# Performance work log

Hardware: AMD Instinct MI355X
Metric: run time of the kernel (lower is better)

The kernel has to match this reference:

```python
import jax, jax.numpy as jnp
import numpy as np

B, N, F, K, O = 4, 4096, 32, 6, 128


def setup_inputs() -> dict:
    key = jax.random.key(0)
    k1, k2, k3, k4 = jax.random.split(key, 4)
    x = jax.random.normal(k1, (B, N, F), dtype=jnp.float32)
    # dense per-batch (normalized-Laplacian-like) operator; scaled for stable recurrence
    L = jax.random.normal(k2, (B, N, N), dtype=jnp.float32) / np.float32(np.sqrt(N))
    # per-order projection weights lins[k]: in -> out  (stored [K, F, O])
    W = jax.random.normal(k3, (K, F, O), dtype=jnp.float32) * 0.1
    # per-order scalar 1x1 'theta' weights lins_theta[k]
    theta = jax.random.normal(k4, (K,), dtype=jnp.float32) * 0.1
    return {"x": x, "L": L, "W": W, "theta": theta}


def reference(x, L, W, theta):
    # Chebyshev recurrence: T0 = x, T1 = L@x, T_k = 2 L@T_{k-1} - T_{k-2}
    # Each order: elementwise scalar theta_k (the 1x1 Linear) then Linear(F->O), summed.
    k_orders = W.shape[0]
    x0 = x                                                   # [B,N,F]
    out = theta[0] * jnp.einsum('bnf,fo->bno', x0, W[0])     # [B,N,O]
    if k_orders > 1:
        x1 = jnp.matmul(L, x0)                               # [B,N,F]
        out = out + theta[1] * jnp.einsum('bnf,fo->bno', x1, W[1])
    for k in range(2, k_orders):
        x2 = 2.0 * jnp.matmul(L, x1) - x0
        out = out + theta[k] * jnp.einsum('bnf,fo->bno', x2, W[k])
        x0, x1 = x1, x2
    return out
```

## Files before the change

kernel.cpp:

```cpp
#include <hip/hip_runtime.h>

#define N4 4096
#define FF 32
#define KK 6
#define OO 128
#define BB 4

typedef __attribute__((ext_vector_type(8))) short  short8;
typedef __attribute__((ext_vector_type(4))) float  f32x4;
typedef __attribute__((ext_vector_type(4))) int    i32x4;
typedef __attribute__((ext_vector_type(2))) unsigned int u32x2;

__device__ __forceinline__ float b2f(unsigned short h) {
    union { float f; unsigned u; } v; v.u = ((unsigned)h) << 16; return v.f;
}
__device__ __forceinline__ unsigned short f2b(float f) {
    union { float f; unsigned u; } v; v.f = f;
    unsigned r = (v.u + 0x7FFFu + ((v.u >> 16) & 1u)) >> 16;
    return (unsigned short)r;
}

__device__ __forceinline__ long tb_idx(int b, int ks, int half, int lane) {
    return ((((long)b * 128 + ks) * 2 + half) * 64 + lane) * 8;
}

__global__ __launch_bounds__(256) void make_wc(const float* __restrict__ W,
                                               const float* __restrict__ theta,
                                               unsigned short* __restrict__ Wc) {
    int idx = blockIdx.x * 256 + threadIdx.x;
    int k = idx >> 12;
    Wc[idx] = f2b(theta[k] * W[idx]);
}

__global__ __launch_bounds__(256) void x_to_t(const float* __restrict__ x,
                                              unsigned short* __restrict__ T0) {
    __shared__ __align__(16) unsigned short Ol[32][72];
    int tid = threadIdx.x, bid = blockIdx.x;
    int b = bid >> 6; int nc = bid & 63; long n0 = (long)nc * 64;
    int nl = tid >> 2, fg = (tid & 3) * 8;
    const float* src = x + ((long)b * N4 + n0 + nl) * FF + fg;
    f32x4 v0 = *(const f32x4*)src;
    f32x4 v1 = *(const f32x4*)(src + 4);
#pragma unroll
    for (int e = 0; e < 4; ++e) {
        Ol[fg + e][nl]     = f2b(v0[e]);
        Ol[fg + 4 + e][nl] = f2b(v1[e]);
    }
    __syncthreads();
    int ks_l = tid >> 7, half = (tid >> 6) & 1, lane = tid & 63;
    int quad = lane >> 4, l16 = lane & 15;
    int f = half * 16 + l16, nloc = ks_l * 32 + quad * 8;
    *(i32x4*)(T0 + tb_idx(b, nc * 2 + ks_l, half, lane)) = *(const i32x4*)&Ol[f][nloc];
}

__device__ __forceinline__ void split_reduce_store(const float (*Pr)[2][64][4],
                                                   int tid, int b, int ms,
                                                   const unsigned short* __restrict__ Tpp,
                                                   unsigned short* __restrict__ Tout,
                                                   float a, float c) {
    if (tid >= 64) return;
    int half = tid >> 5, qi = (tid >> 4) & 1, l16 = tid & 15;
    f32x4 sA = {0.f, 0.f, 0.f, 0.f}, sB = {0.f, 0.f, 0.f, 0.f};
#pragma unroll
    for (int ss = 0; ss < 4; ++ss) {
        f32x4 va = *(const f32x4*)&Pr[ss][half][qi * 32 + l16][0];
        f32x4 vb = *(const f32x4*)&Pr[ss][half][qi * 32 + 16 + l16][0];
#pragma unroll
        for (int e = 0; e < 4; ++e) { sA[e] += va[e]; sB[e] += vb[e]; }
    }
    float vals[8] = {sA[0], sA[1], sA[2], sA[3], sB[0], sB[1], sB[2], sB[3]};
    int lane_o = ((ms & 1) * 2 + qi) * 16 + l16;
    long oidx = tb_idx(b, ms >> 1, half, lane_o);
    i32x4 pk;
    if (Tpp) {
        short8 tv = *(const short8*)(Tpp + oidx);
#pragma unroll
        for (int p = 0; p < 4; ++p)
            pk[p] = (unsigned)f2b(a * vals[2 * p]     + c * b2f((unsigned short)tv[2 * p]))
                  | ((unsigned)f2b(a * vals[2 * p + 1] + c * b2f((unsigned short)tv[2 * p + 1])) << 16);
    } else {
#pragma unroll
        for (int p = 0; p < 4; ++p)
            pk[p] = (unsigned)f2b(a * vals[2 * p])
                  | ((unsigned)f2b(a * vals[2 * p + 1]) << 16);
    }
    *(i32x4*)(Tout + oidx) = pk;
}

__global__ __launch_bounds__(256) void gemm_pass1(const float* __restrict__ L,
                                                  unsigned short* __restrict__ Lb,
                                                  const unsigned short* __restrict__ Tb0,
                                                  unsigned short* __restrict__ Tout) {
    __shared__ __align__(16) unsigned short Sw[4][2][2][64][8];
    __shared__ __align__(16) float Pr[4][2][64][4];
    int tid = threadIdx.x, bid = blockIdx.x;
    int b = bid >> 8, ms = bid & 255;
    int w = tid >> 6, lane = tid & 63, l16 = lane & 15;
    int rgrp = lane >> 4;
    const float* Ls = L + ((long)b * N4 + ms * 16 + rgrp) * N4 + (long)w * 1024 + l16 * 4;
    int ks_loc_w = l16 >> 3, quad_w = (l16 >> 1) & 3, e0 = (l16 & 1) * 4;
    const unsigned short* Bbase = Tb0 + tb_idx(b, w * 32, 0, lane);
    unsigned short* LbBase = Lb + (((long)(b * 256 + ms) * 128 + w * 32) * 64 + lane) * 8;

    f32x4 acc0 = {0.f,0.f,0.f,0.f}, acc1 = {0.f,0.f,0.f,0.f};
    f32x4 v[4], vn[4];
#pragma unroll
    for (int j = 0; j < 4; ++j) v[j] = *(const f32x4*)(Ls + (long)j * 4 * N4);

    for (int it = 0; it < 16; ++it) {
        if (it + 1 < 16) {
#pragma unroll
            for (int j = 0; j < 4; ++j)
                vn[j] = *(const f32x4*)(Ls + (long)j * 4 * N4 + (it + 1) * 64);
        }
        short8 b00 = *(const short8*)(Bbase + (long)(it * 2 + 0) * 1024);
        short8 b01 = *(const short8*)(Bbase + (long)(it * 2 + 0) * 1024 + 512);
        short8 b10 = *(const short8*)(Bbase + (long)(it * 2 + 1) * 1024);
        short8 b11 = *(const short8*)(Bbase + (long)(it * 2 + 1) * 1024 + 512);
        unsigned short* Sb = &Sw[w][it & 1][0][0][0];
#pragma unroll
        for (int j = 0; j < 4; ++j) {
            u32x2 pk;
            pk[0] = (unsigned)f2b(v[j][0]) | ((unsigned)f2b(v[j][1]) << 16);
            pk[1] = (unsigned)f2b(v[j][2]) | ((unsigned)f2b(v[j][3]) << 16);
            int lane_o = quad_w * 16 + j * 4 + rgrp;
            *(u32x2*)(Sb + (ks_loc_w * 64 + lane_o) * 8 + e0) = pk;
        }
#pragma unroll
        for (int h = 0; h < 2; ++h) {
            short8 af = *(const short8*)(Sb + (h * 64 + lane) * 8);
            *(short8*)(LbBase + (long)(it * 2 + h) * 512) = af;
            acc0 = __builtin_amdgcn_mfma_f32_16x16x32_bf16(af, h ? b10 : b00, acc0, 0, 0, 0);
            acc1 = __builtin_amdgcn_mfma_f32_16x16x32_bf16(af, h ? b11 : b01, acc1, 0, 0, 0);
        }
#pragma unroll
        for (int j = 0; j < 4; ++j) v[j] = vn[j];
    }
    *(f32x4*)&Pr[w][0][lane][0] = acc0;
    *(f32x4*)&Pr[w][1][lane][0] = acc1;
    __syncthreads();
    split_reduce_store(Pr, tid, b, ms, nullptr, Tout, 1.f, 0.f);
}

__global__ __launch_bounds__(256) void gemm_frag(const unsigned short* __restrict__ Lb,
                                                 const unsigned short* __restrict__ Tb,
                                                 const unsigned short* __restrict__ Tpp,
                                                 unsigned short* __restrict__ Tout,
                                                 float a, float c) {
    __shared__ __align__(16) float Pr[4][2][64][4];
    int tid = threadIdx.x, bid = blockIdx.x;
    int b = bid >> 8, ms = bid & 255;
    int s = tid >> 6, lane = tid & 63;
    const unsigned short* Ap = Lb + (((long)(b * 256 + ms) * 128 + s * 32) * 64 + lane) * 8;
    const unsigned short* Bp = Tb + tb_idx(b, s * 32, 0, lane);

    f32x4 acc0 = {0.f,0.f,0.f,0.f}, acc1 = {0.f,0.f,0.f,0.f};
    short8 Ar[4], B0r[4], B1r[4];
#pragma unroll
    for (int i = 0; i < 4; ++i) {
        Ar[i]  = *(const short8*)(Ap + (long)i * 512);
        B0r[i] = *(const short8*)(Bp + (long)i * 1024);
        B1r[i] = *(const short8*)(Bp + (long)i * 1024 + 512);
    }
#pragma unroll 4
    for (int ks = 0; ks < 32; ++ks) {
        int sl = ks & 3;
        short8 aa = Ar[sl], b0 = B0r[sl], b1 = B1r[sl];
        if (ks + 4 < 32) {
            Ar[sl]  = *(const short8*)(Ap + (long)(ks + 4) * 512);
            B0r[sl] = *(const short8*)(Bp + (long)(ks + 4) * 1024);
            B1r[sl] = *(const short8*)(Bp + (long)(ks + 4) * 1024 + 512);
        }
        acc0 = __builtin_amdgcn_mfma_f32_16x16x32_bf16(aa, b0, acc0, 0, 0, 0);
        acc1 = __builtin_amdgcn_mfma_f32_16x16x32_bf16(aa, b1, acc1, 0, 0, 0);
    }
    *(f32x4*)&Pr[s][0][lane][0] = acc0;
    *(f32x4*)&Pr[s][1][lane][0] = acc1;
    __syncthreads();
    split_reduce_store(Pr, tid, b, ms, Tpp, Tout, a, c);
}

__global__ __launch_bounds__(256) void proj(const unsigned short* __restrict__ T,
                                            const unsigned short* __restrict__ Wc,
                                            float* __restrict__ out) {
    __shared__ __align__(16) unsigned short Tl[192][72];
    __shared__ __align__(16) unsigned short Wl[192][64];
    int tid = threadIdx.x, bid = blockIdx.x;
    int b = bid >> 7; int rem = bid & 127;
    int nc = rem >> 1; long n0 = (long)nc * 64; int oh = rem & 1;
    const long T_SLOT = (long)BB * FF * N4;
#pragma unroll
    for (int it = 0; it < 6; ++it) {
        int row = it * 32 + (tid >> 3);
        int col = (tid & 7) * 8;
        int k = row >> 5, f = row & 31;
        int ks = nc * 2 + (col >> 5), half = f >> 4;
        int lane = ((col & 31) >> 3) * 16 + (f & 15);
        *(i32x4*)&Tl[row][col] = *(const i32x4*)(T + (long)k * T_SLOT + tb_idx(b, ks, half, lane));
        *(i32x4*)&Wl[row][col] = *(const i32x4*)(Wc + (long)row * OO + oh * 64 + col);
    }
    __syncthreads();
    int ol = tid & 63;
    int nb = (tid >> 6) * 16;
    float acc[16];
#pragma unroll
    for (int r = 0; r < 16; ++r) acc[r] = 0.f;
    for (int kf = 0; kf < 192; ++kf) {
        float w = b2f(Wl[kf][ol]);
#pragma unroll
        for (int rv = 0; rv < 2; ++rv) {
            short8 tv = *(const short8*)&Tl[kf][nb + rv * 8];
#pragma unroll
            for (int e = 0; e < 8; ++e)
                acc[rv * 8 + e] += b2f((unsigned short)tv[e]) * w;
        }
    }
    int o = oh * 64 + ol;
#pragma unroll
    for (int r = 0; r < 16; ++r)
        out[((long)b * N4 + n0 + nb + r) * OO + o] = acc[r];
}

extern "C" void kernel_launch(void* const* d_in, const int* in_sizes, int n_in,
                              void* d_out, int out_size, void* d_ws, size_t ws_size,
                              hipStream_t stream) {
    const float* x     = (const float*)d_in[0];
    const float* L     = (const float*)d_in[1];
    const float* W     = (const float*)d_in[2];
    const float* theta = (const float*)d_in[3];
    float* out = (float*)d_out;
    char* ws = (char*)d_ws;

    const size_t LB_BYTES = (size_t)BB * N4 * N4 * 2;
    const size_t T_SLOT   = (size_t)BB * FF * N4;
    const size_t T_BYTES  = (size_t)KK * T_SLOT * 2;

    unsigned short* Lb = (unsigned short*)ws;
    unsigned short* T  = (unsigned short*)(ws + LB_BYTES);
    unsigned short* Wc = (unsigned short*)(ws + LB_BYTES + T_BYTES);

    make_wc<<<96, 256, 0, stream>>>(W, theta, Wc);
    x_to_t<<<256, 256, 0, stream>>>(x, T);

    gemm_pass1<<<1024, 256, 0, stream>>>(L, Lb, T, T + 1 * T_SLOT);

    for (int k = 2; k < KK; ++k) {
        gemm_frag<<<1024, 256, 0, stream>>>(Lb, T + (k - 1) * T_SLOT,
                                            T + (k - 2) * T_SLOT, T + k * T_SLOT,
                                            2.f, -1.f);
    }

    proj<<<512, 256, 0, stream>>>(T, Wc, out);
}
```

Before: 512.4 us.

## Compute two 16-row tiles per block to reuse T fragments, 8-way K split

After: 507.9 us. About the same (-0.9%).

```diff
diff --git a/kernel.cpp b/kernel.cpp
--- a/kernel.cpp
+++ b/kernel.cpp
@@ -142,42 +142,73 @@
     split_reduce_store(Pr, tid, b, ms, nullptr, Tout, 1.f, 0.f);
 }
 
-__global__ __launch_bounds__(256) void gemm_frag(const unsigned short* __restrict__ Lb,
+__global__ __launch_bounds__(512) void gemm_frag(const unsigned short* __restrict__ Lb,
                                                  const unsigned short* __restrict__ Tb,
                                                  const unsigned short* __restrict__ Tpp,
                                                  unsigned short* __restrict__ Tout,
                                                  float a, float c) {
-    __shared__ __align__(16) float Pr[4][2][64][4];
-    int tid = threadIdx.x, bid = blockIdx.x;
-    int b = bid >> 8, ms = bid & 255;
+    __shared__ __align__(16) float Pr[8][2][2][64][4];
+    int tid = threadIdx.x;
+    int bid = blockIdx.x;
+    bid = (bid & 7) * 64 + (bid >> 3);
+    int b = bid >> 7, m32 = bid & 127;
     int s = tid >> 6, lane = tid & 63;
-    const unsigned short* Ap = Lb + (((long)(b * 256 + ms) * 128 + s * 32) * 64 + lane) * 8;
-    const unsigned short* Bp = Tb + tb_idx(b, s * 32, 0, lane);
-
-    f32x4 acc0 = {0.f,0.f,0.f,0.f}, acc1 = {0.f,0.f,0.f,0.f};
-    short8 Ar[4], B0r[4], B1r[4];
+
+    const unsigned short* Ap0 = Lb + (((long)(b * 256 + m32 * 2 + 0) * 128 + s * 16) * 64 + lane) * 8;
+    const unsigned short* Ap1 = Lb + (((long)(b * 256 + m32 * 2 + 1) * 128 + s * 16) * 64 + lane) * 8;
+    const unsigned short* Bp  = Tb + tb_idx(b, s * 16, 0, lane);
+
+    f32x4 acc00 = {0.f,0.f,0.f,0.f}, acc01 = {0.f,0.f,0.f,0.f};
+    f32x4 acc10 = {0.f,0.f,0.f,0.f}, acc11 = {0.f,0.f,0.f,0.f};
+    short8 A0r[4], A1r[4], B0r[4], B1r[4];
 #pragma unroll
     for (int i = 0; i < 4; ++i) {
-        Ar[i]  = *(const short8*)(Ap + (long)i * 512);
+        A0r[i] = *(const short8*)(Ap0 + (long)i * 512);
+        A1r[i] = *(const short8*)(Ap1 + (long)i * 512);
         B0r[i] = *(const short8*)(Bp + (long)i * 1024);
         B1r[i] = *(const short8*)(Bp + (long)i * 1024 + 512);
     }
-#pragma unroll 4
-    for (int ks = 0; ks < 32; ++ks) {
-        int sl = ks & 3;
-        short8 aa = Ar[sl], b0 = B0r[sl], b1 = B1r[sl];
-        if (ks + 4 < 32) {
-            Ar[sl]  = *(const short8*)(Ap + (long)(ks + 4) * 512);
-            B0r[sl] = *(const short8*)(Bp + (long)(ks + 4) * 1024);
-            B1r[sl] = *(const short8*)(Bp + (long)(ks + 4) * 1024 + 512);
-        }
-        acc0 = __builtin_amdgcn_mfma_f32_16x16x32_bf16(aa, b0, acc0, 0, 0, 0);
-        acc1 = __builtin_amdgcn_mfma_f32_16x16x32_bf16(aa, b1, acc1, 0, 0, 0);
-    }
-    *(f32x4*)&Pr[s][0][lane][0] = acc0;
-    *(f32x4*)&Pr[s][1][lane][0] = acc1;
-    __syncthreads();
-    split_reduce_store(Pr, tid, b, ms, Tpp, Tout, a, c);
+#pragma unroll
+    for (int i = 0; i < 16; ++i) {
+        int sl = i & 3;
+        short8 a0 = A0r[sl], a1 = A1r[sl], b0 = B0r[sl], b1 = B1r[sl];
+        if (i + 4 < 16) {
+            A0r[sl] = *(const short8*)(Ap0 + (long)(i + 4) * 512);
+            A1r[sl] = *(const short8*)(Ap1 + (long)(i + 4) * 512);
+            B0r[sl] = *(const short8*)(Bp + (long)(i + 4) * 1024);
+            B1r[sl] = *(const short8*)(Bp + (long)(i + 4) * 1024 + 512);
+        }
+        acc00 = __builtin_amdgcn_mfma_f32_16x16x32_bf16(a0, b0, acc00, 0, 0, 0);
+        acc01 = __builtin_amdgcn_mfma_f32_16x16x32_bf16(a0, b1, acc01, 0, 0, 0);
+        acc10 = __builtin_amdgcn_mfma_f32_16x16x32_bf16(a1, b0, acc10, 0, 0, 0);
+        acc11 = __builtin_amdgcn_mfma_f32_16x16x32_bf16(a1, b1, acc11, 0, 0, 0);
+    }
+    *(f32x4*)&Pr[s][0][0][lane][0] = acc00;
+    *(f32x4*)&Pr[s][0][1][lane][0] = acc01;
+    *(f32x4*)&Pr[s][1][0][lane][0] = acc10;
+    *(f32x4*)&Pr[s][1][1][lane][0] = acc11;
+    __syncthreads();
+    if (tid >= 128) return;
+    int g = tid >> 6, t = tid & 63;
+    int half = t >> 5, qi = (t >> 4) & 1, l16 = t & 15;
+    f32x4 sA = {0.f,0.f,0.f,0.f}, sB = {0.f,0.f,0.f,0.f};
+#pragma unroll
+    for (int ss = 0; ss < 8; ++ss) {
+        f32x4 va = *(const f32x4*)&Pr[ss][g][half][qi * 32 + l16][0];
+        f32x4 vb = *(const f32x4*)&Pr[ss][g][half][qi * 32 + 16 + l16][0];
+#pragma unroll
+        for (int e = 0; e < 4; ++e) { sA[e] += va[e]; sB[e] += vb[e]; }
+    }
+    float vals[8] = {sA[0], sA[1], sA[2], sA[3], sB[0], sB[1], sB[2], sB[3]};
+    int lane_o = (g * 2 + qi) * 16 + l16;
+    long oidx = tb_idx(b, m32, half, lane_o);
+    short8 tv = *(const short8*)(Tpp + oidx);
+    i32x4 pk;
+#pragma unroll
+    for (int p = 0; p < 4; ++p)
+        pk[p] = (unsigned)f2b(a * vals[2 * p]     + c * b2f((unsigned short)tv[2 * p]))
+              | ((unsigned)f2b(a * vals[2 * p + 1] + c * b2f((unsigned short)tv[2 * p + 1])) << 16);
+    *(i32x4*)(Tout + oidx) = pk;
 }
 
 __global__ __launch_bounds__(256) void proj(const unsigned short* __restrict__ T,
@@ -245,9 +276,9 @@
     gemm_pass1<<<1024, 256, 0, stream>>>(L, Lb, T, T + 1 * T_SLOT);
 
     for (int k = 2; k < KK; ++k) {
-        gemm_frag<<<1024, 256, 0, stream>>>(Lb, T + (k - 1) * T_SLOT,
-                                            T + (k - 2) * T_SLOT, T + k * T_SLOT,
-                                            2.f, -1.f);
+        gemm_frag<<<512, 512, 0, stream>>>(Lb, T + (k - 1) * T_SLOT,
+                                           T + (k - 2) * T_SLOT, T + k * T_SLOT,
+                                           2.f, -1.f);
     }
 
     proj<<<512, 256, 0, stream>>>(T, Wc, out);
```

## Split L transcode into standalone kernel and deepen gemm_frag prefetch

Applied to the files above, without the earlier changes.

New measurement: 533.4 us. 4.1% more time.

```diff
diff --git a/kernel.cpp b/kernel.cpp
--- a/kernel.cpp
+++ b/kernel.cpp
@@ -9,7 +9,6 @@
 typedef __attribute__((ext_vector_type(8))) short  short8;
 typedef __attribute__((ext_vector_type(4))) float  f32x4;
 typedef __attribute__((ext_vector_type(4))) int    i32x4;
-typedef __attribute__((ext_vector_type(2))) unsigned int u32x2;
 
 __device__ __forceinline__ float b2f(unsigned short h) {
     union { float f; unsigned u; } v; v.u = ((unsigned)h) << 16; return v.f;
@@ -51,6 +50,37 @@
     int quad = lane >> 4, l16 = lane & 15;
     int f = half * 16 + l16, nloc = ks_l * 32 + quad * 8;
     *(i32x4*)(T0 + tb_idx(b, nc * 2 + ks_l, half, lane)) = *(const i32x4*)&Ol[f][nloc];
+}
+
+__global__ __launch_bounds__(256) void lb_transcode(const float* __restrict__ L,
+                                                    unsigned short* __restrict__ Lb) {
+    int tid = threadIdx.x, bid = blockIdx.x;
+    int b = bid >> 9, rem = bid & 511;
+    int ms = rem >> 1, hk = rem & 1;
+    int w = tid >> 6, lane = tid & 63;
+    const float* Ls = L + ((long)b * N4 + ms * 16 + (lane & 15)) * N4 + (lane >> 4) * 8;
+    int ks0 = hk * 64 + w * 16;
+    unsigned short* dst = Lb + ((long)((b * 256 + ms) * 128 + ks0)) * 512 + lane * 8;
+#pragma unroll
+    for (int bt = 0; bt < 2; ++bt) {
+        f32x4 v[16];
+#pragma unroll
+        for (int i = 0; i < 8; ++i) {
+            int col = (ks0 + bt * 8 + i) * 32;
+            v[2 * i]     = *(const f32x4*)(Ls + col);
+            v[2 * i + 1] = *(const f32x4*)(Ls + col + 4);
+        }
+#pragma unroll
+        for (int i = 0; i < 8; ++i) {
+            i32x4 pk;
+#pragma unroll
+            for (int p = 0; p < 2; ++p) {
+                pk[p]     = (unsigned)f2b(v[2 * i][2 * p])     | ((unsigned)f2b(v[2 * i][2 * p + 1]) << 16);
+                pk[p + 2] = (unsigned)f2b(v[2 * i + 1][2 * p]) | ((unsigned)f2b(v[2 * i + 1][2 * p + 1]) << 16);
+            }
+            *(i32x4*)(dst + (long)(bt * 8 + i) * 512) = pk;
+        }
+    }
 }
 
 __device__ __forceinline__ void split_reduce_store(const float (*Pr)[2][64][4],
@@ -87,61 +117,6 @@
     *(i32x4*)(Tout + oidx) = pk;
 }
 
-__global__ __launch_bounds__(256) void gemm_pass1(const float* __restrict__ L,
-                                                  unsigned short* __restrict__ Lb,
-                                                  const unsigned short* __restrict__ Tb0,
-                                                  unsigned short* __restrict__ Tout) {
-    __shared__ __align__(16) unsigned short Sw[4][2][2][64][8];
-    __shared__ __align__(16) float Pr[4][2][64][4];
-    int tid = threadIdx.x, bid = blockIdx.x;
-    int b = bid >> 8, ms = bid & 255;
-    int w = tid >> 6, lane = tid & 63, l16 = lane & 15;
-    int rgrp = lane >> 4;
-    const float* Ls = L + ((long)b * N4 + ms * 16 + rgrp) * N4 + (long)w * 1024 + l16 * 4;
-    int ks_loc_w = l16 >> 3, quad_w = (l16 >> 1) & 3, e0 = (l16 & 1) * 4;
-    const unsigned short* Bbase = Tb0 + tb_idx(b, w * 32, 0, lane);
-    unsigned short* LbBase = Lb + (((long)(b * 256 + ms) * 128 + w * 32) * 64 + lane) * 8;
-
-    f32x4 acc0 = {0.f,0.f,0.f,0.f}, acc1 = {0.f,0.f,0.f,0.f};
-    f32x4 v[4], vn[4];
-#pragma unroll
-    for (int j = 0; j < 4; ++j) v[j] = *(const f32x4*)(Ls + (long)j * 4 * N4);
-
-    for (int it = 0; it < 16; ++it) {
-        if (it + 1 < 16) {
-#pragma unroll
-            for (int j = 0; j < 4; ++j)
-                vn[j] = *(const f32x4*)(Ls + (long)j * 4 * N4 + (it + 1) * 64);
-        }
-        short8 b00 = *(const short8*)(Bbase + (long)(it * 2 + 0) * 1024);
-        short8 b01 = *(const short8*)(Bbase + (long)(it * 2 + 0) * 1024 + 512);
-        short8 b10 = *(const short8*)(Bbase + (long)(it * 2 + 1) * 1024);
-        short8 b11 = *(const short8*)(Bbase + (long)(it * 2 + 1) * 1024 + 512);
-        unsigned short* Sb = &Sw[w][it & 1][0][0][0];
-#pragma unroll
-        for (int j = 0; j < 4; ++j) {
-            u32x2 pk;
-            pk[0] = (unsigned)f2b(v[j][0]) | ((unsigned)f2b(v[j][1]) << 16);
-            pk[1] = (unsigned)f2b(v[j][2]) | ((unsigned)f2b(v[j][3]) << 16);
-            int lane_o = quad_w * 16 + j * 4 + rgrp;
-            *(u32x2*)(Sb + (ks_loc_w * 64 + lane_o) * 8 + e0) = pk;
-        }
-#pragma unroll
-        for (int h = 0; h < 2; ++h) {
-            short8 af = *(const short8*)(Sb + (h * 64 + lane) * 8);
-            *(short8*)(LbBase + (long)(it * 2 + h) * 512) = af;
-            acc0 = __builtin_amdgcn_mfma_f32_16x16x32_bf16(af, h ? b10 : b00, acc0, 0, 0, 0);
-            acc1 = __builtin_amdgcn_mfma_f32_16x16x32_bf16(af, h ? b11 : b01, acc1, 0, 0, 0);
-        }
-#pragma unroll
-        for (int j = 0; j < 4; ++j) v[j] = vn[j];
-    }
-    *(f32x4*)&Pr[w][0][lane][0] = acc0;
-    *(f32x4*)&Pr[w][1][lane][0] = acc1;
-    __syncthreads();
-    split_reduce_store(Pr, tid, b, ms, nullptr, Tout, 1.f, 0.f);
-}
-
 __global__ __launch_bounds__(256) void gemm_frag(const unsigned short* __restrict__ Lb,
                                                  const unsigned short* __restrict__ Tb,
                                                  const unsigned short* __restrict__ Tpp,
@@ -155,21 +130,21 @@
     const unsigned short* Bp = Tb + tb_idx(b, s * 32, 0, lane);
 
     f32x4 acc0 = {0.f,0.f,0.f,0.f}, acc1 = {0.f,0.f,0.f,0.f};
-    short8 Ar[4], B0r[4], B1r[4];
-#pragma unroll
-    for (int i = 0; i < 4; ++i) {
+    short8 Ar[8], B0r[8], B1r[8];
+#pragma unroll
+    for (int i = 0; i < 8; ++i) {
         Ar[i]  = *(const short8*)(Ap + (long)i * 512);
         B0r[i] = *(const short8*)(Bp + (long)i * 1024);
         B1r[i] = *(const short8*)(Bp + (long)i * 1024 + 512);
     }
-#pragma unroll 4
+#pragma unroll
     for (int ks = 0; ks < 32; ++ks) {
-        int sl = ks & 3;
+        int sl = ks & 7;
         short8 aa = Ar[sl], b0 = B0r[sl], b1 = B1r[sl];
-        if (ks + 4 < 32) {
-            Ar[sl]  = *(const short8*)(Ap + (long)(ks + 4) * 512);
-            B0r[sl] = *(const short8*)(Bp + (long)(ks + 4) * 1024);
-            B1r[sl] = *(const short8*)(Bp + (long)(ks + 4) * 1024 + 512);
+        if (ks + 8 < 32) {
+            Ar[sl]  = *(const short8*)(Ap + (long)(ks + 8) * 512);
+            B0r[sl] = *(const short8*)(Bp + (long)(ks + 8) * 1024);
+            B1r[sl] = *(const short8*)(Bp + (long)(ks + 8) * 1024 + 512);
         }
         acc0 = __builtin_amdgcn_mfma_f32_16x16x32_bf16(aa, b0, acc0, 0, 0, 0);
         acc1 = __builtin_amdgcn_mfma_f32_16x16x32_bf16(aa, b1, acc1, 0, 0, 0);
@@ -242,7 +217,9 @@
     make_wc<<<96, 256, 0, stream>>>(W, theta, Wc);
     x_to_t<<<256, 256, 0, stream>>>(x, T);
 
-    gemm_pass1<<<1024, 256, 0, stream>>>(L, Lb, T, T + 1 * T_SLOT);
+    lb_transcode<<<2048, 256, 0, stream>>>(L, Lb);
+
+    gemm_frag<<<1024, 256, 0, stream>>>(Lb, T, nullptr, T + T_SLOT, 1.f, 0.f);
 
     for (int k = 2; k < KK; ++k) {
         gemm_frag<<<1024, 256, 0, stream>>>(Lb, T + (k - 1) * T_SLOT,
```
